# Performance work log

Hardware: AMD Instinct MI355X
Metric: run time of the kernel (lower is better)

The kernel has to match this reference:

```python
import jax, jax.numpy as jnp
import numpy as np

N_HEADS = 4

def setup_inputs() -> dict:
    key = jax.random.key(0)
    ks = jax.random.split(key, 9)
    B, C, H, W = 4, 256, 64, 64
    nh, hs = N_HEADS, C // N_HEADS
    s = 0.02
    return {
        "x": jax.random.normal(ks[0], (B, C, H, W), jnp.float32),
        "wq": jax.random.normal(ks[1], (C, C), jnp.float32) * s,
        "bq": jax.random.normal(ks[2], (C,), jnp.float32) * s,
        "wk": jax.random.normal(ks[3], (C, C), jnp.float32) * s,
        "bk": jax.random.normal(ks[4], (C,), jnp.float32) * s,
        "wv": jax.random.normal(ks[5], (C, C), jnp.float32) * s,
        "bv": jax.random.normal(ks[6], (C,), jnp.float32) * s,
        "rel_h": jax.random.normal(ks[7], (1, nh, hs, 1, H), jnp.float32),
        "rel_w": jax.random.normal(ks[8], (1, nh, hs, W, 1), jnp.float32),
    }

def reference(x, wq, bq, wk, bk, wv, bv, rel_h, rel_w):
    B, C, H, W = x.shape
    nh = N_HEADS
    hs = C // nh
    S = H * W

    def proj(w, b):
        # 1x1 conv == per-pixel linear over channels -> [B, C, H, W]
        y = jnp.einsum('oc,bchw->bohw', w, x) + b[None, :, None, None]
        # faithful to torch .view: flatten [C,H,W] row-major into [S, nh, hs]
        y = y.reshape(B, S, nh, hs)
        return y.transpose(0, 2, 1, 3)  # [B, nh, S, hs]

    q = proj(wq, bq)
    k = proj(wk, bk)
    v = proj(wv, bv)

    # content scores (NOTE: no 1/sqrt(d) scaling in BoT override)
    attn_content = jnp.einsum('bnqd,bnkd->bnqk', q, k)  # [B, nh, S, S]
    # learned relative position term: broadcast-add then flatten (w,h) order
    pos = (rel_h + rel_w).reshape(1, nh, hs, S)  # [1, nh, hs, S]
    attn_position = jnp.einsum('bnqd,ands->bnqs', q, pos)  # [B, nh, S, S]

    probs = jax.nn.softmax(attn_content + attn_position, axis=-1)
    ctx = jnp.einsum('bnqk,bnkd->bnqd', probs, v)  # [B, nh, S, hs]
    # faithful to torch: transpose(1,2) then view(B, C, width, height)
    out = ctx.transpose(0, 2, 1, 3).reshape(B, C, W, H)
    return out
```

## Files before the change

kernel.cpp:

```cpp
#include <hip/hip_runtime.h>
#include <hip/hip_bf16.h>
#include <stdint.h>
#include <math.h>

typedef __bf16 bf16_t;
typedef __bf16 bf16x8 __attribute__((ext_vector_type(8)));
typedef float  f32x4  __attribute__((ext_vector_type(4)));
typedef float  f32x16 __attribute__((ext_vector_type(16)));
typedef unsigned int u32;

#define S_SZ 4096
#define HS   64
#define OUT_B_STRIDE (256 * 64 * 64)
#define LOG2E 1.4426950408889634f

#define GLOAD_LDS(gsrc, ldst)                                                              \
    __builtin_amdgcn_global_load_lds((__attribute__((address_space(1))) void*)(void*)(gsrc), \
                                     (__attribute__((address_space(3))) void*)(void*)(ldst),  \
                                     16, 0, 0)

static __device__ __forceinline__ u32 pack2(__bf16 a, __bf16 b) {
    return (u32)__builtin_bit_cast(uint16_t, a) | ((u32)__builtin_bit_cast(uint16_t, b) << 16);
}

__global__ __launch_bounds__(256)
void wprep_kernel(const float* __restrict__ wq, const float* __restrict__ wk,
                  const float* __restrict__ wv, bf16_t* __restrict__ Wh,
                  bf16_t* __restrict__ Wl)
{
    const int o = blockIdx.x;
    const int c = threadIdx.x;
    const float* src = o < 256 ? wq : (o < 512 ? wk : wv);
    float v = src[(size_t)(o & 255) * 256 + c];
    if (o < 256) v *= LOG2E;
    __bf16 h = (__bf16)v;
    Wh[(size_t)o * 256 + c] = h;
    Wl[(size_t)o * 256 + c] = (__bf16)(v - (float)h);
}

__global__ __launch_bounds__(512, 2)
void proj_kernel(const float* __restrict__ x,
                 const bf16_t* __restrict__ Wh, const bf16_t* __restrict__ Wl,
                 const float* __restrict__ bq, const float* __restrict__ bk,
                 const float* __restrict__ bv,
                 const float* __restrict__ rel_h, const float* __restrict__ rel_w,
                 bf16_t* __restrict__ q_ws, bf16_t* __restrict__ k2_ws,
                 bf16_t* __restrict__ vt2_ws)
{
    const int bx = blockIdx.x;
    const int b  = bx >> 6;
    const int h  = bx & 63;
    const int p0 = h * 64;
    const int n  = h & 3;
    const int h2 = h >> 2;
    const int bn = b * 4 + n;
    const int tid = threadIdx.x;

    __shared__ __align__(16) bf16_t XT[2][64 * 256];

    {
        const int cpair = tid & 127, pg = tid >> 7;
        const int c0 = cpair * 2;
        const float* x0 = x + ((size_t)b * 256 + c0) * 4096 + p0 + pg * 16;
        const int sub = (c0 >> 6) * 128;
        const int u   = (c0 >> 3) & 7;
        const int e2  = (c0 & 7) * 2;
        #pragma unroll
        for (int i4 = 0; i4 < 4; ++i4) {
            f32x4 ra = *(const f32x4*)(x0 + i4 * 4);
            f32x4 rb = *(const f32x4*)(x0 + 4096 + i4 * 4);
            #pragma unroll
            for (int i = 0; i < 4; ++i) {
                const int p = pg * 16 + i4 * 4 + i;
                __bf16 ha = (__bf16)ra[i], hb = (__bf16)rb[i];
                float  la = ra[i] - (float)ha, lb = rb[i] - (float)hb;
                const int off = p * 512 + sub + ((u ^ (p & 7)) * 16) + e2;
                *(u32*)((char*)&XT[0][0] + off) = pack2(ha, hb);
                *(u32*)((char*)&XT[1][0] + off) = pack2((__bf16)la, (__bf16)lb);
            }
        }
    }
    __syncthreads();

    const int wid = tid >> 6, lane = tid & 63, l31 = lane & 31, hi = lane >> 5;

    int obs[3], pjs[3];
    const bf16_t* whp[3];
    const bf16_t* wlp[3];
    #pragma unroll
    for (int j = 0; j < 3; ++j) {
        const int of = (wid * 3 + j) * 32;
        pjs[j] = of >> 8;
        obs[j] = of & 255;
        whp[j] = Wh + (size_t)(of + l31) * 256 + hi * 8;
        wlp[j] = Wl + (size_t)(of + l31) * 256 + hi * 8;
    }

    const char* XHp = (const char*)&XT[0][0] + l31 * 512;
    const char* XLp = (const char*)&XT[1][0] + l31 * 512;

    f32x16 acc[3][2] = {};

    #pragma unroll
    for (int ks = 0; ks < 16; ++ks) {
        bf16x8 wh[3], wl[3];
        #pragma unroll
        for (int j = 0; j < 3; ++j) {
            wh[j] = *(const bf16x8*)(whp[j] + ks * 16);
            wl[j] = *(const bf16x8*)(wlp[j] + ks * 16);
        }
        const int rb_ = (ks >> 2) * 128 + ((((ks * 2 + hi) & 7) ^ (l31 & 7)) * 16);
        bf16x8 xh[2], xl[2];
        #pragma unroll
        for (int pt = 0; pt < 2; ++pt) {
            xh[pt] = *(const bf16x8*)(XHp + pt * 16384 + rb_);
            xl[pt] = *(const bf16x8*)(XLp + pt * 16384 + rb_);
        }
        #pragma unroll
        for (int j = 0; j < 3; ++j)
            #pragma unroll
            for (int pt = 0; pt < 2; ++pt) {
                acc[j][pt] = __builtin_amdgcn_mfma_f32_32x32x16_bf16(wh[j], xh[pt], acc[j][pt], 0, 0, 0);
                acc[j][pt] = __builtin_amdgcn_mfma_f32_32x32x16_bf16(wh[j], xl[pt], acc[j][pt], 0, 0, 0);
                acc[j][pt] = __builtin_amdgcn_mfma_f32_32x32x16_bf16(wl[j], xh[pt], acc[j][pt], 0, 0, 0);
            }
    }

    #pragma unroll
    for (int j = 0; j < 3; ++j) {
        const int ob_ = obs[j];
        const float* bp = pjs[j] == 0 ? bq : (pjs[j] == 1 ? bk : bv);
        f32x4 bv4[4];
        #pragma unroll
        for (int g2 = 0; g2 < 4; ++g2) {
            bv4[g2] = *(const f32x4*)(bp + ob_ + hi * 4 + g2 * 8);
            if (pjs[j] == 0) {
                #pragma unroll
                for (int i = 0; i < 4; ++i) bv4[g2][i] *= LOG2E;
            }
        }

        #pragma unroll
        for (int pt = 0; pt < 2; ++pt) {
            const int d = pt * 32 + l31;
            if (pjs[j] == 0) {
                bf16_t* qp = q_ws + ((size_t)bn * 4096) * 64 + d;
                #pragma unroll
                for (int g2 = 0; g2 < 4; ++g2)
                    #pragma unroll
                    for (int rr = 0; rr < 4; ++rr) {
                        const int o = ob_ + rr + 4 * hi + 8 * g2;
                        const int s = o * 16 + h2;
                        qp[(size_t)s * 64] = (bf16_t)(acc[j][pt][g2 * 4 + rr] + bv4[g2][rr]);
                    }
            } else if (pjs[j] == 1) {
                const float* rhp = rel_h + (n * 64 + d) * 64;
                const float* rwp = rel_w + (n * 64 + d) * 64;
                bf16_t* kp = k2_ws + ((size_t)bn * 4096) * 64 + d;
                #pragma unroll
                for (int g2 = 0; g2 < 4; ++g2)
                    #pragma unroll
                    for (int rr = 0; rr < 4; ++rr) {
                        const int o = ob_ + rr + 4 * hi + 8 * g2;
                        const int t = h2 * 256 + o;
                        const float r = rhp[(o & 3) * 16 + h2] + rwp[o >> 2];
                        kp[(size_t)t * 64] = (bf16_t)(acc[j][pt][g2 * 4 + rr] + bv4[g2][rr] + r);
                    }
            } else {
                bf16_t* vp = vt2_ws + ((size_t)bn * 64 + d) * 4096;
                #pragma unroll
                for (int g2 = 0; g2 < 4; ++g2) {
                    const int t4 = h2 * 256 + ob_ + 4 * hi + 8 * g2;
                    ushort4 pk;
                    pk.x = __builtin_bit_cast(uint16_t, (__bf16)(acc[j][pt][g2 * 4 + 0] + bv4[g2][0]));
                    pk.y = __builtin_bit_cast(uint16_t, (__bf16)(acc[j][pt][g2 * 4 + 1] + bv4[g2][1]));
                    pk.z = __builtin_bit_cast(uint16_t, (__bf16)(acc[j][pt][g2 * 4 + 2] + bv4[g2][2]));
                    pk.w = __builtin_bit_cast(uint16_t, (__bf16)(acc[j][pt][g2 * 4 + 3] + bv4[g2][3]));
                    *(ushort4*)(vp + t4) = pk;
                }
            }
        }
    }
}

__global__ __launch_bounds__(512, 2)
void attn_kernel(const bf16_t* __restrict__ q_ws, const bf16_t* __restrict__ k_ws,
                 const bf16_t* __restrict__ vt_ws, float* __restrict__ out)
{
    const int tid  = threadIdx.x;
    const int wid  = tid >> 6;
    const int lane = tid & 63;
    const int l31  = lane & 31;
    const int hi   = lane >> 5;

    const int wg  = blockIdx.x;
    const int swz = (wg & 7) * 32 + (wg >> 3);
    const int bn  = swz >> 4;
    const int qb  = swz & 15;
    const int b   = bn >> 2, n = bn & 3;

    __shared__ __align__(16) bf16_t Kt[4][64 * 64];
    __shared__ __align__(16) bf16_t Vt[4][64 * 64];

    const bf16_t* Qb = q_ws  + (size_t)bn * S_SZ * HS;
    const bf16_t* Kb = k_ws  + (size_t)bn * S_SZ * HS;
    const bf16_t* Vb = vt_ws + (size_t)bn * HS * S_SZ;

    const int c0 = wid * 64 + lane;
    const int ra = c0 >> 3, sa = c0 & 7;
    const int ga = sa ^ (ra & 7);
    const bf16_t* ksrc = Kb + ra * HS + ga * 8;
    const bf16_t* vsrc = Vb + (size_t)ra * S_SZ + ga * 8;

    const int q = qb * 256 + wid * 32 + l31;
    bf16x8 qf[4];
    #pragma unroll
    for (int dk = 0; dk < 4; ++dk)
        qf[dk] = *(const bf16x8*)(Qb + (size_t)q * HS + dk * 16 + hi * 8);

    f32x16 oacc[2];
    f32x16 Z16;
    #pragma unroll
    for (int i = 0; i < 16; ++i) { oacc[0][i] = 0.f; oacc[1][i] = 0.f; Z16[i] = 0.f; }
    float lsum = 0.f;

    const int swzme = (l31 & 7) << 4;

    #pragma unroll
    for (int p = 0; p < 3; ++p) {
        GLOAD_LDS(ksrc + (size_t)p * 64 * HS, &Kt[p][wid * 512]);
        GLOAD_LDS(vsrc + p * 64,              &Vt[p][wid * 512]);
    }
    asm volatile("s_waitcnt vmcnt(4)" ::: "memory");
    __builtin_amdgcn_s_barrier();
    asm volatile("" ::: "memory");

    for (int tb = 0; tb < 64; tb += 4) {
        #pragma unroll
        for (int u = 0; u < 4; ++u) {
            const int t = tb + u;
            {
                const int ts = (t + 3 > 63) ? 63 : t + 3;
                GLOAD_LDS(ksrc + (size_t)ts * 64 * HS, &Kt[(u + 3) & 3][wid * 512]);
                GLOAD_LDS(vsrc + ts * 64,              &Vt[(u + 3) & 3][wid * 512]);
            }

            const char* Kbase = (const char*)&Kt[u][0] + l31 * 128;
            const char* Vbase = (const char*)&Vt[u][0] + l31 * 128;

            f32x16 sacc[2];
            __builtin_amdgcn_s_setprio(1);
            #pragma unroll
            for (int hh = 0; hh < 2; ++hh) {
                bf16x8 kf[4];
                #pragma unroll
                for (int dk = 0; dk < 4; ++dk)
                    kf[dk] = *(const bf16x8*)(Kbase + hh * 4096 + (((2 * dk + hi) * 16) ^ swzme));
                sacc[hh] = __builtin_amdgcn_mfma_f32_32x32x16_bf16(kf[0], qf[0], Z16, 0, 0, 0);
                #pragma unroll
                for (int dk = 1; dk < 4; ++dk)
                    sacc[hh] = __builtin_amdgcn_mfma_f32_32x32x16_bf16(kf[dk], qf[dk], sacc[hh], 0, 0, 0);
            }
            __builtin_amdgcn_s_setprio(0);

            u32 Wd[2][4][2];
            float ps[4] = {0.f, 0.f, 0.f, 0.f};
            #pragma unroll
            for (int hh = 0; hh < 2; ++hh)
                #pragma unroll
                for (int c = 0; c < 4; ++c)
                    #pragma unroll
                    for (int tt = 0; tt < 2; ++tt) {
                        float pa = __builtin_amdgcn_exp2f(sacc[hh][c * 4 + tt * 2]);
                        float pb = __builtin_amdgcn_exp2f(sacc[hh][c * 4 + tt * 2 + 1]);
                        ps[c] += pa + pb;
                        u32 w;
                        asm("v_cvt_pk_bf16_f32 %0, %1, %2" : "=v"(w) : "v"(pa), "v"(pb));
                        Wd[hh][c][tt] = w;
                    }
            lsum += (ps[0] + ps[1]) + (ps[2] + ps[3]);

            u32 F[4][4];
            #pragma unroll
            for (int hh = 0; hh < 2; ++hh)
                #pragma unroll
                for (int pr = 0; pr < 2; ++pr)
                    #pragma unroll
                    for (int tt = 0; tt < 2; ++tt) {
                        u32 a = Wd[hh][2 * pr][tt], bb = Wd[hh][2 * pr + 1][tt];
                        asm("v_permlane32_swap_b32 %0, %1" : "+v"(a), "+v"(bb));
                        F[2 * hh + pr][tt]     = a;
                        F[2 * hh + pr][2 + tt] = bb;
                    }

            __builtin_amdgcn_s_setprio(1);
            #pragma unroll
            for (int dh = 0; dh < 2; ++dh) {
                #pragma unroll
                for (int kk = 0; kk < 4; ++kk) {
                    bf16x8 vf = *(const bf16x8*)(Vbase + dh * 4096 + (((2 * kk + hi) * 16) ^ swzme));
                    union { u32 u[4]; bf16x8 v; } pf;
                    pf.u[0] = F[kk][0]; pf.u[1] = F[kk][1];
                    pf.u[2] = F[kk][2]; pf.u[3] = F[kk][3];
                    oacc[dh] = __builtin_amdgcn_mfma_f32_32x32x16_bf16(vf, pf.v, oacc[dh], 0, 0, 0);
                }
            }
            __builtin_amdgcn_s_setprio(0);

            asm volatile("s_waitcnt vmcnt(4)" ::: "memory");
            __builtin_amdgcn_s_barrier();
            asm volatile("" ::: "memory");
        }
    }

    float lt  = lsum + __shfl_xor(lsum, 32);
    float inv = 1.0f / lt;
    float* outp = out + (size_t)b * OUT_B_STRIDE + (size_t)q * 256 + n * 64;
    #pragma unroll
    for (int dh = 0; dh < 2; ++dh)
        #pragma unroll
        for (int g2 = 0; g2 < 4; ++g2) {
            f32x4 v4;
            #pragma unroll
            for (int r = 0; r < 4; ++r) v4[r] = oacc[dh][g2 * 4 + r] * inv;
            *(f32x4*)(outp + dh * 32 + g2 * 8 + hi * 4) = v4;
        }
}

extern "C" void kernel_launch(void* const* d_in, const int* in_sizes, int n_in,
                              void* d_out, int out_size, void* d_ws, size_t ws_size,
                              hipStream_t stream)
{
    const float* x     = (const float*)d_in[0];
    const float* wq    = (const float*)d_in[1];
    const float* bq    = (const float*)d_in[2];
    const float* wk    = (const float*)d_in[3];
    const float* bk    = (const float*)d_in[4];
    const float* wv    = (const float*)d_in[5];
    const float* bv    = (const float*)d_in[6];
    const float* rel_h = (const float*)d_in[7];
    const float* rel_w = (const float*)d_in[8];
    float* out = (float*)d_out;

    bf16_t* q_ws   = (bf16_t*)d_ws;
    bf16_t* k2_ws  = q_ws  + (size_t)16 * S_SZ * HS;
    bf16_t* vt2_ws = k2_ws + (size_t)16 * S_SZ * HS;

    bf16_t* wtail = (bf16_t*)d_out + (size_t)out_size * 2 - (size_t)2 * 768 * 256;
    bf16_t* Wh = wtail;
    bf16_t* Wl = wtail + 768 * 256;

    wprep_kernel<<<768, 256, 0, stream>>>(wq, wk, wv, Wh, Wl);
    proj_kernel<<<256, 512, 0, stream>>>(x, Wh, Wl, bq, bk, bv, rel_h, rel_w,
                                         q_ws, k2_ws, vt2_ws);
    attn_kernel<<<256, 512, 0, stream>>>(q_ws, k2_ws, vt2_ws, out);
}
```

Measured before the change: 137.0 us.

## Stage projection outputs through LDS, precompute rel-pos table, halve attention blocks

The projection kernel now writes Q, V and K tiles into shared memory and copies them out with 16-byte coalesced global stores, replacing scattered 2-byte stores. The rel_h+rel_w positional sum is precomputed once into a bf16 table by the prep kernel and added during the K store. The attention kernel drops to 256 threads per block over 512 blocks of 128 queries, with each wave issuing twice as many K/V loads. The extra barriers and LDS round trips add overhead, and the positional term is now rounded to bf16 before it is added to K, which slightly changes precision.

Measured after the change: 129.0 us. 5.9% less time.

```diff
diff --git a/kernel.cpp b/kernel.cpp
--- a/kernel.cpp
+++ b/kernel.cpp
@@ -24,26 +24,40 @@
 }
 
 __global__ __launch_bounds__(256)
-void wprep_kernel(const float* __restrict__ wq, const float* __restrict__ wk,
-                  const float* __restrict__ wv, bf16_t* __restrict__ Wh,
-                  bf16_t* __restrict__ Wl)
+void prep_kernel(const float* __restrict__ wq, const float* __restrict__ wk,
+                 const float* __restrict__ wv, const float* __restrict__ rel_h,
+                 const float* __restrict__ rel_w,
+                 bf16_t* __restrict__ Wh, bf16_t* __restrict__ Wl,
+                 bf16_t* __restrict__ Rt)
 {
-    const int o = blockIdx.x;
-    const int c = threadIdx.x;
-    const float* src = o < 256 ? wq : (o < 512 ? wk : wv);
-    float v = src[(size_t)(o & 255) * 256 + c];
-    if (o < 256) v *= LOG2E;
-    __bf16 h = (__bf16)v;
-    Wh[(size_t)o * 256 + c] = h;
-    Wl[(size_t)o * 256 + c] = (__bf16)(v - (float)h);
+    const int blk = blockIdx.x;
+    if (blk < 768) {
+        const int o = blk;
+        const int c = threadIdx.x;
+        const float* src = o < 256 ? wq : (o < 512 ? wk : wv);
+        float v = src[(size_t)(o & 255) * 256 + c];
+        if (o < 256) v *= LOG2E;
+        __bf16 h = (__bf16)v;
+        Wh[(size_t)o * 256 + c] = h;
+        Wl[(size_t)o * 256 + c] = (__bf16)(v - (float)h);
+    } else {
+        const int e = (blk - 768) * 256 + threadIdx.x;
+        const int n  = e >> 18;
+        const int rr = e & 262143;
+        const int t  = rr >> 6;
+        const int d  = rr & 63;
+        const int h2 = t >> 8, o = t & 255;
+        float v = rel_h[(n * 64 + d) * 64 + (o & 3) * 16 + h2]
+                + rel_w[(n * 64 + d) * 64 + (o >> 2)];
+        Rt[e] = (bf16_t)v;
+    }
 }
 
 __global__ __launch_bounds__(512, 2)
 void proj_kernel(const float* __restrict__ x,
                  const bf16_t* __restrict__ Wh, const bf16_t* __restrict__ Wl,
                  const float* __restrict__ bq, const float* __restrict__ bk,
-                 const float* __restrict__ bv,
-                 const float* __restrict__ rel_h, const float* __restrict__ rel_w,
+                 const float* __restrict__ bv, const bf16_t* __restrict__ Rt,
                  bf16_t* __restrict__ q_ws, bf16_t* __restrict__ k2_ws,
                  bf16_t* __restrict__ vt2_ws)
 {
@@ -56,7 +70,7 @@
     const int bn = b * 4 + n;
     const int tid = threadIdx.x;
 
-    __shared__ __align__(16) bf16_t XT[2][64 * 256];
+    __shared__ __align__(16) char SM[65536];
 
     {
         const int cpair = tid & 127, pg = tid >> 7;
@@ -75,8 +89,8 @@
                 __bf16 ha = (__bf16)ra[i], hb = (__bf16)rb[i];
                 float  la = ra[i] - (float)ha, lb = rb[i] - (float)hb;
                 const int off = p * 512 + sub + ((u ^ (p & 7)) * 16) + e2;
-                *(u32*)((char*)&XT[0][0] + off) = pack2(ha, hb);
-                *(u32*)((char*)&XT[1][0] + off) = pack2((__bf16)la, (__bf16)lb);
+                *(u32*)(SM + off)         = pack2(ha, hb);
+                *(u32*)(SM + 32768 + off) = pack2((__bf16)la, (__bf16)lb);
             }
         }
     }
@@ -96,8 +110,8 @@
         wlp[j] = Wl + (size_t)(of + l31) * 256 + hi * 8;
     }
 
-    const char* XHp = (const char*)&XT[0][0] + l31 * 512;
-    const char* XLp = (const char*)&XT[1][0] + l31 * 512;
+    const char* XHp = SM + l31 * 512;
+    const char* XLp = SM + 32768 + l31 * 512;
 
     f32x16 acc[3][2] = {};
 
@@ -125,65 +139,99 @@
                 acc[j][pt] = __builtin_amdgcn_mfma_f32_32x32x16_bf16(wl[j], xh[pt], acc[j][pt], 0, 0, 0);
             }
     }
-
+    __syncthreads();
+
+    f32x4 bias[3][2][4];
     #pragma unroll
     for (int j = 0; j < 3; ++j) {
-        const int ob_ = obs[j];
         const float* bp = pjs[j] == 0 ? bq : (pjs[j] == 1 ? bk : bv);
-        f32x4 bv4[4];
         #pragma unroll
         for (int g2 = 0; g2 < 4; ++g2) {
-            bv4[g2] = *(const f32x4*)(bp + ob_ + hi * 4 + g2 * 8);
+            f32x4 v = *(const f32x4*)(bp + obs[j] + hi * 4 + g2 * 8);
             if (pjs[j] == 0) {
                 #pragma unroll
-                for (int i = 0; i < 4; ++i) bv4[g2][i] *= LOG2E;
-            }
-        }
-
+                for (int i = 0; i < 4; ++i) v[i] *= LOG2E;
+            }
+            bias[j][0][g2] = v;  bias[j][1][g2] = v;
+        }
+    }
+
+    #pragma unroll
+    for (int j = 0; j < 3; ++j) {
+        if (pjs[j] == 1) continue;
         #pragma unroll
         for (int pt = 0; pt < 2; ++pt) {
             const int d = pt * 32 + l31;
-            if (pjs[j] == 0) {
-                bf16_t* qp = q_ws + ((size_t)bn * 4096) * 64 + d;
-                #pragma unroll
-                for (int g2 = 0; g2 < 4; ++g2)
-                    #pragma unroll
-                    for (int rr = 0; rr < 4; ++rr) {
-                        const int o = ob_ + rr + 4 * hi + 8 * g2;
-                        const int s = o * 16 + h2;
-                        qp[(size_t)s * 64] = (bf16_t)(acc[j][pt][g2 * 4 + rr] + bv4[g2][rr]);
+            #pragma unroll
+            for (int g2 = 0; g2 < 4; ++g2)
+                #pragma unroll
+                for (int rr = 0; rr < 4; ++rr) {
+                    const int o = obs[j] + rr + 4 * hi + 8 * g2;
+                    const float v = acc[j][pt][g2 * 4 + rr] + bias[j][pt][g2][rr];
+                    if (pjs[j] == 0) {
+                        *(bf16_t*)(SM + o * 128 + d * 2) = (bf16_t)v;
+                    } else {
+                        *(bf16_t*)(SM + 32768 + d * 512 + ((o * 2) ^ ((d & 7) << 4))) = (bf16_t)v;
                     }
-            } else if (pjs[j] == 1) {
-                const float* rhp = rel_h + (n * 64 + d) * 64;
-                const float* rwp = rel_w + (n * 64 + d) * 64;
-                bf16_t* kp = k2_ws + ((size_t)bn * 4096) * 64 + d;
-                #pragma unroll
-                for (int g2 = 0; g2 < 4; ++g2)
-                    #pragma unroll
-                    for (int rr = 0; rr < 4; ++rr) {
-                        const int o = ob_ + rr + 4 * hi + 8 * g2;
-                        const int t = h2 * 256 + o;
-                        const float r = rhp[(o & 3) * 16 + h2] + rwp[o >> 2];
-                        kp[(size_t)t * 64] = (bf16_t)(acc[j][pt][g2 * 4 + rr] + bv4[g2][rr] + r);
-                    }
-            } else {
-                bf16_t* vp = vt2_ws + ((size_t)bn * 64 + d) * 4096;
-                #pragma unroll
-                for (int g2 = 0; g2 < 4; ++g2) {
-                    const int t4 = h2 * 256 + ob_ + 4 * hi + 8 * g2;
-                    ushort4 pk;
-                    pk.x = __builtin_bit_cast(uint16_t, (__bf16)(acc[j][pt][g2 * 4 + 0] + bv4[g2][0]));
-                    pk.y = __builtin_bit_cast(uint16_t, (__bf16)(acc[j][pt][g2 * 4 + 1] + bv4[g2][1]));
-                    pk.z = __builtin_bit_cast(uint16_t, (__bf16)(acc[j][pt][g2 * 4 + 2] + bv4[g2][2]));
-                    pk.w = __builtin_bit_cast(uint16_t, (__bf16)(acc[j][pt][g2 * 4 + 3] + bv4[g2][3]));
-                    *(ushort4*)(vp + t4) = pk;
                 }
-            }
+        }
+    }
+    __syncthreads();
+    {
+        bf16_t* qp = q_ws + (size_t)bn * 4096 * 64;
+        #pragma unroll
+        for (int i = 0; i < 4; ++i) {
+            const int c = i * 512 + tid;
+            const int o = c >> 3, d8 = c & 7;
+            uint4 v = *(const uint4*)(SM + c * 16);
+            *(uint4*)(qp + (size_t)(o * 16 + h2) * 64 + d8 * 8) = v;
+        }
+        bf16_t* vp = vt2_ws + (size_t)bn * 64 * 4096 + h2 * 256;
+        #pragma unroll
+        for (int i = 0; i < 4; ++i) {
+            const int c = i * 512 + tid;
+            const int d = c >> 5, k = c & 31;
+            uint4 v = *(const uint4*)(SM + 32768 + d * 512 + ((k * 16) ^ ((d & 7) << 4)));
+            *(uint4*)(vp + (size_t)d * 4096 + k * 8) = v;
+        }
+    }
+    __syncthreads();
+
+    #pragma unroll
+    for (int j = 0; j < 3; ++j) {
+        if (pjs[j] != 1) continue;
+        #pragma unroll
+        for (int pt = 0; pt < 2; ++pt) {
+            const int d = pt * 32 + l31;
+            #pragma unroll
+            for (int g2 = 0; g2 < 4; ++g2)
+                #pragma unroll
+                for (int rr = 0; rr < 4; ++rr) {
+                    const int o = obs[j] + rr + 4 * hi + 8 * g2;
+                    *(bf16_t*)(SM + o * 128 + d * 2) =
+                        (bf16_t)(acc[j][pt][g2 * 4 + rr] + bias[j][pt][g2][rr]);
+                }
+        }
+    }
+    __syncthreads();
+    {
+        const bf16_t* Rp = Rt + ((size_t)n * 4096 + h2 * 256) * 64;
+        bf16_t* kp = k2_ws + ((size_t)bn * 4096 + h2 * 256) * 64;
+        #pragma unroll
+        for (int i = 0; i < 4; ++i) {
+            const int c = i * 512 + tid;
+            bf16x8 kv = *(const bf16x8*)(SM + c * 16);
+            bf16x8 rv = *(const bf16x8*)(Rp + c * 8);
+            bf16x8 res;
+            #pragma unroll
+            for (int ii = 0; ii < 8; ++ii)
+                res[ii] = (__bf16)((float)kv[ii] + (float)rv[ii]);
+            *(bf16x8*)(kp + c * 8) = res;
         }
     }
 }
 
-__global__ __launch_bounds__(512, 2)
+__global__ __launch_bounds__(256, 2)
 void attn_kernel(const bf16_t* __restrict__ q_ws, const bf16_t* __restrict__ k_ws,
                  const bf16_t* __restrict__ vt_ws, float* __restrict__ out)
 {
@@ -194,9 +242,9 @@
     const int hi   = lane >> 5;
 
     const int wg  = blockIdx.x;
-    const int swz = (wg & 7) * 32 + (wg >> 3);
-    const int bn  = swz >> 4;
-    const int qb  = swz & 15;
+    const int swz = (wg & 7) * 64 + (wg >> 3);
+    const int bn  = swz >> 5;
+    const int qb  = swz & 31;
     const int b   = bn >> 2, n = bn & 3;
 
     __shared__ __align__(16) bf16_t Kt[4][64 * 64];
@@ -207,12 +255,19 @@
     const bf16_t* Vb = vt_ws + (size_t)bn * HS * S_SZ;
 
     const int c0 = wid * 64 + lane;
-    const int ra = c0 >> 3, sa = c0 & 7;
-    const int ga = sa ^ (ra & 7);
-    const bf16_t* ksrc = Kb + ra * HS + ga * 8;
-    const bf16_t* vsrc = Vb + (size_t)ra * S_SZ + ga * 8;
-
-    const int q = qb * 256 + wid * 32 + l31;
+    const int ra = c0 >> 3, ga = (c0 & 7) ^ (ra & 7);
+    const bf16_t* ksrcA = Kb + ra * HS + ga * 8;
+    const bf16_t* ksrcB = ksrcA + 32 * HS;
+    const bf16_t* vsrcA = Vb + (size_t)ra * S_SZ + ga * 8;
+    const bf16_t* vsrcB = vsrcA + (size_t)32 * S_SZ;
+
+#define STAGE(buf, ts)                                                        \
+    GLOAD_LDS(ksrcA + (size_t)(ts) * 64 * HS, &Kt[buf][wid * 512]);           \
+    GLOAD_LDS(ksrcB + (size_t)(ts) * 64 * HS, &Kt[buf][2048 + wid * 512]);    \
+    GLOAD_LDS(vsrcA + (ts) * 64,              &Vt[buf][wid * 512]);           \
+    GLOAD_LDS(vsrcB + (ts) * 64,              &Vt[buf][2048 + wid * 512]);
+
+    const int q = qb * 128 + wid * 32 + l31;
     bf16x8 qf[4];
     #pragma unroll
     for (int dk = 0; dk < 4; ++dk)
@@ -226,12 +281,8 @@
 
     const int swzme = (l31 & 7) << 4;
 
-    #pragma unroll
-    for (int p = 0; p < 3; ++p) {
-        GLOAD_LDS(ksrc + (size_t)p * 64 * HS, &Kt[p][wid * 512]);
-        GLOAD_LDS(vsrc + p * 64,              &Vt[p][wid * 512]);
-    }
-    asm volatile("s_waitcnt vmcnt(4)" ::: "memory");
+    STAGE(0, 0); STAGE(1, 1); STAGE(2, 2);
+    asm volatile("s_waitcnt vmcnt(8)" ::: "memory");
     __builtin_amdgcn_s_barrier();
     asm volatile("" ::: "memory");
 
@@ -241,8 +292,7 @@
             const int t = tb + u;
             {
                 const int ts = (t + 3 > 63) ? 63 : t + 3;
-                GLOAD_LDS(ksrc + (size_t)ts * 64 * HS, &Kt[(u + 3) & 3][wid * 512]);
-                GLOAD_LDS(vsrc + ts * 64,              &Vt[(u + 3) & 3][wid * 512]);
+                STAGE((u + 3) & 3, ts);
             }
 
             const char* Kbase = (const char*)&Kt[u][0] + l31 * 128;
@@ -307,11 +357,12 @@
             }
             __builtin_amdgcn_s_setprio(0);
 
-            asm volatile("s_waitcnt vmcnt(4)" ::: "memory");
+            asm volatile("s_waitcnt vmcnt(8)" ::: "memory");
             __builtin_amdgcn_s_barrier();
             asm volatile("" ::: "memory");
         }
     }
+#undef STAGE
 
     float lt  = lsum + __shfl_xor(lsum, 32);
     float inv = 1.0f / lt;
@@ -346,12 +397,13 @@
     bf16_t* k2_ws  = q_ws  + (size_t)16 * S_SZ * HS;
     bf16_t* vt2_ws = k2_ws + (size_t)16 * S_SZ * HS;
 
-    bf16_t* wtail = (bf16_t*)d_out + (size_t)out_size * 2 - (size_t)2 * 768 * 256;
-    bf16_t* Wh = wtail;
-    bf16_t* Wl = wtail + 768 * 256;
-
-    wprep_kernel<<<768, 256, 0, stream>>>(wq, wk, wv, Wh, Wl);
-    proj_kernel<<<256, 512, 0, stream>>>(x, Wh, Wl, bq, bk, bv, rel_h, rel_w,
+    bf16_t* end = (bf16_t*)d_out + (size_t)out_size * 2;
+    bf16_t* Wl  = end - 196608;
+    bf16_t* Wh  = Wl - 196608;
+    bf16_t* Rt  = Wh - 1048576;
+
+    prep_kernel<<<4864, 256, 0, stream>>>(wq, wk, wv, rel_h, rel_w, Wh, Wl, Rt);
+    proj_kernel<<<256, 512, 0, stream>>>(x, Wh, Wl, bq, bk, bv, Rt,
                                          q_ws, k2_ws, vt2_ws);
-    attn_kernel<<<256, 512, 0, stream>>>(q_ws, k2_ws, vt2_ws, out);
+    attn_kernel<<<512, 256, 0, stream>>>(q_ws, k2_ws, vt2_ws, out);
 }
```
